# Performance work log

Hardware: AMD Instinct MI355X
Metric: run time of the kernel (lower is better)

The kernel has to match this reference:

```python
import jax, jax.numpy as jnp
import numpy as np

B, W, N, K = 8, 16, 40, 10
DN = DL = 128
DE = 128
H = 4
NEG_SLOPE = 0.2


def _build_graph():
    # per-graph ring adjacency: i -> (i+d) % N for d=1..K, in dense_to_sparse order (src-major, dst ascending)
    src0, dst0 = [], []
    for i in range(N):
        ds = sorted(((i + d) % N) for d in range(1, K + 1))
        src0 += [i] * K
        dst0 += ds
    src0 = np.asarray(src0)
    dst0 = np.asarray(dst0)
    G = B * W
    Epg = N * K
    offs = np.arange(G)[:, None] * N
    node_adj = np.stack([(src0[None] + offs).reshape(-1), (dst0[None] + offs).reshape(-1)])
    # line graph: for each node, pair every incoming edge with every outgoing edge (torch repeat/tile order)
    a0, a1, fe = [], [], []
    for num in range(N):
        inc = np.nonzero(dst0 == num)[0]
        out = np.nonzero(src0 == num)[0]
        a0.append(np.repeat(inc, out.size))
        a1.append(np.tile(out, inc.size))
        fe.append(np.full(inc.size * out.size, num))
    a0, a1, fe = np.concatenate(a0), np.concatenate(a1), np.concatenate(fe)
    keep = a0 != a1  # remove_self_loops (no-op here, kept for fidelity)
    a0, a1, fe = a0[keep], a1[keep], fe[keep]
    eoffs = np.arange(G)[:, None] * Epg
    edge_adj = np.stack([(a0[None] + eoffs).reshape(-1), (a1[None] + eoffs).reshape(-1)])
    edge_efea = (fe[None] + offs).reshape(-1)
    return node_adj, edge_adj, edge_efea


def setup_inputs() -> dict:
    key = jax.random.key(0)
    node_adj, edge_adj, edge_efea = _build_graph()
    Epg = N * K
    D1 = DN + DL
    ks = jax.random.split(key, 16)

    def lin(k, fi, fo):
        return jax.random.normal(k, (fi, fo), jnp.float32) / np.sqrt(fi).astype(np.float32)

    return dict(
        x_node=jax.random.normal(ks[0], (B, W, N, DN), jnp.float32),
        x_trace=jax.random.normal(ks[1], (B, W, Epg, DE), jnp.float32),
        x_log=jax.random.normal(ks[2], (B, W, N, DL), jnp.float32),
        node_adj=jnp.asarray(node_adj, jnp.int32),
        edge_adj=jnp.asarray(edge_adj, jnp.int32),
        edge_efea=jnp.asarray(edge_efea, jnp.int32),
        Wl1=lin(ks[3], D1, D1), bl1=jnp.zeros((D1,), jnp.float32),
        Wr1=lin(ks[4], D1, D1), br1=jnp.zeros((D1,), jnp.float32),
        We1=lin(ks[5], DE, D1), be1=jnp.zeros((D1,), jnp.float32),
        att1=jax.random.normal(ks[6], (H, D1 // H), jnp.float32) / np.sqrt(D1 // H).astype(np.float32),
        bias1=jnp.zeros((D1,), jnp.float32),
        Wl2=lin(ks[7], DE, DE), bl2=jnp.zeros((DE,), jnp.float32),
        Wr2=lin(ks[8], DE, DE), br2=jnp.zeros((DE,), jnp.float32),
        We2=lin(ks[9], D1, DE), be2=jnp.zeros((DE,), jnp.float32),
        att2=jax.random.normal(ks[10], (H, DE // H), jnp.float32) / np.sqrt(DE // H).astype(np.float32),
        bias2=jnp.zeros((DE,), jnp.float32),
    )


def _gatv2(x, edge_index, edge_attr, Wl, bl, Wr, br, We, be, att, bias, heads):
    """PyG GATv2Conv (eval mode, add_self_loops=False, concat heads)."""
    n = x.shape[0]
    HC = Wl.shape[1]
    C = HC // heads
    xl = (x @ Wl + bl).reshape(n, heads, C)  # source transform
    xr = (x @ Wr + br).reshape(n, heads, C)  # target transform
    src, dst = edge_index[0], edge_index[1]
    ea = (edge_attr @ We + be).reshape(-1, heads, C)
    m = jax.nn.leaky_relu(xl[src] + xr[dst] + ea, NEG_SLOPE)  # [E,H,C]
    logits = jnp.einsum('ehc,hc->eh', m, att)
    # segment softmax over incoming edges per target node
    mx = jax.ops.segment_max(logits, dst, num_segments=n)
    mx = jnp.where(jnp.isfinite(mx), mx, 0.0)
    ex = jnp.exp(logits - mx[dst])
    den = jax.ops.segment_sum(ex, dst, num_segments=n)
    alpha = ex / (den[dst] + 1e-16)
    out = jax.ops.segment_sum(alpha[:, :, None] * xl[src], dst, num_segments=n)  # [n,H,C]
    return out.reshape(n, HC) + bias


def reference(x_node, x_trace, x_log, node_adj, edge_adj, edge_efea,
              Wl1, bl1, Wr1, br1, We1, be1, att1, bias1,
              Wl2, bl2, Wr2, br2, We2, be2, att2, bias2):
    b, w, n, dn = x_node.shape
    dl = x_log.shape[-1]
    node = jnp.concatenate([x_node, x_log], axis=-1).reshape(-1, dn + dl)  # [G*N, Dn+Dl]
    trace = x_trace.reshape(-1, x_trace.shape[-1])                          # [G*Epg, De]
    node = _gatv2(node, node_adj, trace, Wl1, bl1, Wr1, br1, We1, be1, att1, bias1, H)
    trace = _gatv2(trace, edge_adj, node[edge_efea], Wl2, bl2, Wr2, br2, We2, be2, att2, bias2, H)
    x_node_o = node[:, :dn].reshape(b, w, n, dn)
    x_trace_o = trace.reshape(b, w, -1, trace.shape[-1])
    x_log_o = node[:, dn:].reshape(b, w, n, dl)
    return (x_node_o, x_trace_o, x_log_o)
```

## Files before the change

### kernel.cpp

```cpp
#include <hip/hip_runtime.h>
#include <hip/hip_bf16.h>

#define D1 256
#define DE 128
#define KDEG 10
#define NPG 40
#define EPG 400
#define LOG2E 1.44269504088896340736f

typedef __attribute__((ext_vector_type(8))) short short8;
typedef __attribute__((ext_vector_type(4))) float f32x4;

static inline int cdiv(size_t a, int b) { return (int)((a + b - 1) / b); }
static inline size_t al256(size_t x) { return (x + 255) & ~(size_t)255; }

__device__ __forceinline__ short f2b(float x) {
  __hip_bfloat16 h = __float2bfloat16(x);
  return *reinterpret_cast<short*>(&h);
}

__device__ __forceinline__ short8 cvt8(const float* __restrict__ src) {
  float4 v0 = *(const float4*)src;
  float4 v1 = *(const float4*)(src + 4);
  short8 t;
  t[0] = f2b(v0.x); t[1] = f2b(v0.y); t[2] = f2b(v0.z); t[3] = f2b(v0.w);
  t[4] = f2b(v1.x); t[5] = f2b(v1.y); t[6] = f2b(v1.z); t[7] = f2b(v1.w);
  return t;
}

__global__ __launch_bounds__(256) void k_setup(const float* __restrict__ xn,
                                               const float* __restrict__ xlg,
                                               const float* __restrict__ xtr,
                                               const float* __restrict__ Wl1,
                                               const float* __restrict__ Wr1,
                                               const float* __restrict__ We1,
                                               const float* __restrict__ Wl2,
                                               const float* __restrict__ Wr2,
                                               const float* __restrict__ We2,
                                               const float* __restrict__ bl1,
                                               const float* __restrict__ br1,
                                               const float* __restrict__ be1,
                                               const float* __restrict__ bl2,
                                               const float* __restrict__ br2,
                                               const int* __restrict__ adj,
                                               int* __restrict__ cnt,
                                               int* __restrict__ inc,
                                               short* __restrict__ Xb,
                                               short* __restrict__ xtr_b,
                                               short* __restrict__ WT12,
                                               short* __restrict__ WTall,
                                               short* __restrict__ We2T,
                                               float* __restrict__ blr1,
                                               float* __restrict__ bfull,
                                               int NN, int NE) {
  size_t idx = (size_t)blockIdx.x * 256 + threadIdx.x;
  size_t n;
  n = (size_t)NN * 32;
  if (idx < n) {
    int row = (int)(idx >> 5), q = (int)(idx & 31);
    const float* src = (q < 16) ? &xn[(size_t)row * 128 + q * 8]
                                : &xlg[(size_t)row * 128 + (q - 16) * 8];
    *(short8*)&Xb[(size_t)row * 256 + q * 8] = cvt8(src);
    return;
  }
  idx -= n;
  n = (size_t)NE * 16;
  if (idx < n) {
    *(short8*)&xtr_b[idx * 8] = cvt8(&xtr[idx * 8]);
    return;
  }
  idx -= n;
  n = 512 * 256;
  if (idx < n) {
    int nn = (int)(idx >> 8), k = (int)(idx & 255);
    float v = (nn < 256) ? Wl1[(size_t)k * 256 + nn] : Wr1[(size_t)k * 256 + (nn - 256)];
    WT12[idx] = f2b(v);
    return;
  }
  idx -= n;
  n = 512 * 128;
  if (idx < n) {
    int nn = (int)(idx >> 7), k = (int)(idx & 127);
    float v;
    if (nn < 256)      v = We1[(size_t)k * 256 + nn];
    else if (nn < 384) v = Wl2[(size_t)k * 128 + (nn - 256)];
    else               v = Wr2[(size_t)k * 128 + (nn - 384)];
    WTall[idx] = f2b(v);
    return;
  }
  idx -= n;
  n = 128 * 256;
  if (idx < n) {
    int nn = (int)(idx >> 8), k = (int)(idx & 255);
    We2T[idx] = f2b(We2[(size_t)k * 128 + nn]);
    return;
  }
  idx -= n;
  n = 512;
  if (idx < n) { blr1[idx] = (idx < 256) ? bl1[idx] : br1[idx - 256]; return; }
  idx -= n;
  n = 512;
  if (idx < n) {
    bfull[idx] = (idx < 256) ? be1[idx] : (idx < 384 ? bl2[idx - 256] : br2[idx - 384]);
    return;
  }
  idx -= n;
  n = (size_t)NE;
  if (idx < n) {
    int dst = adj[NE + idx];
    int slot = atomicAdd(&cnt[dst], 1);
    inc[dst * KDEG + slot] = (int)idx;
  }
}

__global__ __launch_bounds__(256) void k_gemm_dual(const short* __restrict__ Xb,
                                                   const short* __restrict__ WT12,
                                                   const float* __restrict__ blr1,
                                                   float* __restrict__ xlr1,
                                                   const short* __restrict__ xtr_b,
                                                   const short* __restrict__ WTl2,
                                                   const float* __restrict__ bia2,
                                                   float* __restrict__ pool2,
                                                   int NN, int NE) {
  __shared__ __align__(16) short As[64][40];
  __shared__ __align__(16) short Bs[64][40];
  const int tid = threadIdx.x;
  const int wave = tid >> 6, lane = tid & 63;
  const int quad = lane >> 4, l16 = lane & 15;
  const short *A, *WT;
  const float* bias;
  float* C;
  int K, N, m0, n0;
  {
    int bid = blockIdx.x;
    if (bid < 8 * (NN / 64)) {
      A = Xb; WT = WT12; bias = blr1; C = xlr1; K = 256; N = 512;
      n0 = (bid & 7) * 64; m0 = (bid >> 3) * 64;
    } else {
      bid -= 8 * (NN / 64);
      A = xtr_b; WT = WTl2; bias = bia2; C = pool2; K = 128; N = 256;
      n0 = (bid & 3) * 64; m0 = (bid >> 2) * 64;
    }
  }
  const int wm = (wave & 1) * 32, wn = (wave >> 1) * 32;
  const int r = tid >> 2, kc = (tid & 3) << 3;
  f32x4 acc[2][2] = {};
  short8 pa = *(const short8*)&A[(size_t)(m0 + r) * K + kc];
  short8 pb = *(const short8*)&WT[(size_t)(n0 + r) * K + kc];
  for (int k0 = 0; k0 < K; k0 += 32) {
    *(short8*)&As[r][kc] = pa;
    *(short8*)&Bs[r][kc] = pb;
    __syncthreads();
    if (k0 + 32 < K) {
      pa = *(const short8*)&A[(size_t)(m0 + r) * K + (k0 + 32 + kc)];
      pb = *(const short8*)&WT[(size_t)(n0 + r) * K + (k0 + 32 + kc)];
    }
    short8 af[2], bf[2];
    #pragma unroll
    for (int mt = 0; mt < 2; ++mt)
      af[mt] = *(const short8*)&As[wm + mt * 16 + l16][quad << 3];
    #pragma unroll
    for (int nt = 0; nt < 2; ++nt)
      bf[nt] = *(const short8*)&Bs[wn + nt * 16 + l16][quad << 3];
    #pragma unroll
    for (int mt = 0; mt < 2; ++mt)
      #pragma unroll
      for (int nt = 0; nt < 2; ++nt)
        acc[mt][nt] = __builtin_amdgcn_mfma_f32_16x16x32_bf16(
            af[mt], bf[nt], acc[mt][nt], 0, 0, 0);
    __syncthreads();
  }
  #pragma unroll
  for (int nt = 0; nt < 2; ++nt) {
    int col = n0 + wn + nt * 16 + l16;
    float bs = bias[col];
    #pragma unroll
    for (int mt = 0; mt < 2; ++mt) {
      int row = m0 + wm + mt * 16 + (quad << 2);
      #pragma unroll
      for (int rr = 0; rr < 2 * 2; ++rr)
        if (rr < 4) C[(size_t)(row + rr) * N + col] = acc[mt][nt][rr] + bs;
    }
  }
}

__global__ __launch_bounds__(256) void k_gemm_mfma64(const short* __restrict__ A,
                                                     const short* __restrict__ WT,
                                                     const float* __restrict__ bias,
                                                     float* __restrict__ C,
                                                     int M, int K, int N) {
  __shared__ __align__(16) short As[64][40];
  __shared__ __align__(16) short Bs[64][40];
  const int tid = threadIdx.x;
  const int wave = tid >> 6, lane = tid & 63;
  const int quad = lane >> 4, l16 = lane & 15;
  const int m0 = blockIdx.y * 64, n0 = blockIdx.x * 64;
  const int wm = (wave & 1) * 32, wn = (wave >> 1) * 32;
  const int r = tid >> 2, kc = (tid & 3) << 3;
  f32x4 acc[2][2] = {};
  short8 pa = *(const short8*)&A[(size_t)(m0 + r) * K + kc];
  short8 pb = *(const short8*)&WT[(size_t)(n0 + r) * K + kc];
  for (int k0 = 0; k0 < K; k0 += 32) {
    *(short8*)&As[r][kc] = pa;
    *(short8*)&Bs[r][kc] = pb;
    __syncthreads();
    if (k0 + 32 < K) {
      pa = *(const short8*)&A[(size_t)(m0 + r) * K + (k0 + 32 + kc)];
      pb = *(const short8*)&WT[(size_t)(n0 + r) * K + (k0 + 32 + kc)];
    }
    short8 af[2], bf[2];
    #pragma unroll
    for (int mt = 0; mt < 2; ++mt)
      af[mt] = *(const short8*)&As[wm + mt * 16 + l16][quad << 3];
    #pragma unroll
    for (int nt = 0; nt < 2; ++nt)
      bf[nt] = *(const short8*)&Bs[wn + nt * 16 + l16][quad << 3];
    #pragma unroll
    for (int mt = 0; mt < 2; ++mt)
      #pragma unroll
      for (int nt = 0; nt < 2; ++nt)
        acc[mt][nt] = __builtin_amdgcn_mfma_f32_16x16x32_bf16(
            af[mt], bf[nt], acc[mt][nt], 0, 0, 0);
    __syncthreads();
  }
  #pragma unroll
  for (int nt = 0; nt < 2; ++nt) {
    int col = n0 + wn + nt * 16 + l16;
    float bs = bias[col];
    #pragma unroll
    for (int mt = 0; mt < 2; ++mt) {
      int row = m0 + wm + mt * 16 + (quad << 2);
      #pragma unroll
      for (int rr = 0; rr < 4; ++rr)
        C[(size_t)(row + rr) * N + col] = acc[mt][nt][rr] + bs;
    }
  }
}

__global__ __launch_bounds__(256) void k_logit(const short* __restrict__ A,
                                               const short* __restrict__ WT,
                                               const float* __restrict__ bfull,
                                               const float* __restrict__ att1,
                                               const int* __restrict__ adj,
                                               const float* __restrict__ xlr1,
                                               float* __restrict__ logit1,
                                               int NE) {
  const int K = 128;
  struct SmemGemm { short As[128][40]; short Bs[64][40]; };
  struct SmemEpi  { int sdst[128]; float sxl[14][68]; float sxr[NPG][68]; };
  __shared__ __align__(16) union { SmemGemm g; SmemEpi e; } sm;
  const int tid = threadIdx.x;
  const int wave = tid >> 6, lane = tid & 63;
  const int quad = lane >> 4, l16 = lane & 15;
  int bid = blockIdx.x;
  int l = (bid & 7) * ((int)gridDim.x >> 3) + (bid >> 3);
  const int n0 = (l & 3) << 6;
  const int m0 = (l >> 2) << 7;
  const int wm = wave * 32;
  const int ra0 = tid >> 2, ra1 = ra0 + 64;
  const int kc = (tid & 3) << 3;
  f32x4 acc[2][4] = {};
  short8 pa0 = *(const short8*)&A[(size_t)(m0 + ra0) * K + kc];
  short8 pa1 = *(const short8*)&A[(size_t)(m0 + ra1) * K + kc];
  short8 pb  = *(const short8*)&WT[(size_t)(n0 + ra0) * K + kc];
  for (int k0 = 0; k0 < K; k0 += 32) {
    *(short8*)&sm.g.As[ra0][kc] = pa0;
    *(short8*)&sm.g.As[ra1][kc] = pa1;
    *(short8*)&sm.g.Bs[ra0][kc] = pb;
    __syncthreads();
    if (k0 + 32 < K) {
      pa0 = *(const short8*)&A[(size_t)(m0 + ra0) * K + (k0 + 32 + kc)];
      pa1 = *(const short8*)&A[(size_t)(m0 + ra1) * K + (k0 + 32 + kc)];
      pb  = *(const short8*)&WT[(size_t)(n0 + ra0) * K + (k0 + 32 + kc)];
    }
    short8 af[2], bf[4];
    #pragma unroll
    for (int mt = 0; mt < 2; ++mt)
      af[mt] = *(const short8*)&sm.g.As[wm + mt * 16 + l16][quad << 3];
    #pragma unroll
    for (int nt = 0; nt < 4; ++nt)
      bf[nt] = *(const short8*)&sm.g.Bs[nt * 16 + l16][quad << 3];
    #pragma unroll
    for (int mt = 0; mt < 2; ++mt)
      #pragma unroll
      for (int nt = 0; nt < 4; ++nt)
        acc[mt][nt] = __builtin_amdgcn_mfma_f32_16x16x32_bf16(
            af[mt], bf[nt], acc[mt][nt], 0, 0, 0);
    __syncthreads();
  }
  const int gl = m0 / EPG;
  const int gh = (m0 + 127) / EPG;
  const int slo = m0 / KDEG;
  const int nrl = (m0 + 127) / KDEG - slo + 1;
  if (tid < 128) sm.e.sdst[tid] = adj[NE + m0 + tid];
  for (int s = tid; s < nrl * 64; s += 256) {
    int row = s >> 6, c = s & 63;
    sm.e.sxl[row][c] = xlr1[(size_t)(slo + row) * 512 + n0 + c];
  }
  const int h = n0 >> 6;
  float attv[4], bev[4];
  int ccl[4];
  #pragma unroll
  for (int nt = 0; nt < 4; ++nt) {
    int col = n0 + nt * 16 + l16;
    ccl[nt] = col - n0;
    attv[nt] = att1[col] * LOG2E;
    bev[nt] = bfull[col];
  }
  for (int g = gl; g <= gh; ++g) {
    __syncthreads();
    for (int s = tid; s < NPG * 64; s += 256) {
      int row = s >> 6, c = s & 63;
      sm.e.sxr[row][c] = xlr1[(size_t)(g * NPG + row) * 512 + 256 + n0 + c];
    }
    __syncthreads();
    const int elo = g * EPG, ehi = elo + EPG;
    #pragma unroll
    for (int mt = 0; mt < 2; ++mt) {
      #pragma unroll
      for (int r = 0; r < 4; ++r) {
        int le = wm + mt * 16 + (quad << 2) + r;
        int e = m0 + le;
        if (e < elo || e >= ehi) continue;
        int srow = e / KDEG - slo;
        int d = sm.e.sdst[le];
        int drow = d - g * NPG;
        float p = 0.f;
        #pragma unroll
        for (int nt = 0; nt < 4; ++nt) {
          float v = acc[mt][nt][r] + bev[nt] + sm.e.sxl[srow][ccl[nt]]
                  + sm.e.sxr[drow][ccl[nt]];
          v = (v > 0.f) ? v : 0.2f * v;
          p += v * attv[nt];
        }
        p += __shfl_xor(p, 1, 64);
        p += __shfl_xor(p, 2, 64);
        p += __shfl_xor(p, 4, 64);
        p += __shfl_xor(p, 8, 64);
        if (l16 == 0) {
          logit1[(size_t)e * 4 + h] = exp2f(p);
        }
      }
    }
  }
}

__global__ __launch_bounds__(256) void k_agg1(const int* __restrict__ adj,
                                              const int* __restrict__ inc,
                                              const float* __restrict__ xlr1,
                                              const float* __restrict__ logit1,
                                              const float* __restrict__ bias1,
                                              short* __restrict__ nodeoutb,
                                              float* __restrict__ out_node,
                                              float* __restrict__ out_log) {
  int u = blockIdx.x, c = threadIdx.x;
  __shared__ int se[KDEG], ssrc[KDEG];
  __shared__ float slg[KDEG * 4];
  if (c < KDEG) se[c] = inc[u * KDEG + c];
  __syncthreads();
  if (c < KDEG) ssrc[c] = adj[se[c]];
  else if (c >= 64 && c < 64 + KDEG * 4) {
    int t = c - 64;
    slg[t] = logit1[(size_t)se[t >> 2] * 4 + (t & 3)];
  }
  __syncthreads();
  int h = c >> 6;
  float den = 0.f;
  #pragma unroll
  for (int j = 0; j < KDEG; ++j) den += slg[j * 4 + h];
  float rden = 1.f / (den + 1e-16f);
  float acc = 0.f;
  #pragma unroll
  for (int j = 0; j < KDEG; ++j)
    acc += slg[j * 4 + h] * xlr1[(size_t)ssrc[j] * 512 + c];
  float val = acc * rden + bias1[c];
  nodeoutb[(size_t)u * D1 + c] = f2b(val);
  if (c < 128) out_node[(size_t)u * 128 + c] = val;
  else         out_log[(size_t)u * 128 + (c - 128)] = val;
}

__global__ __launch_bounds__(256) void k_gat2_v4(const int* __restrict__ eadj,
                                                 const int* __restrict__ efea,
                                                 const float* __restrict__ pool2,
                                                 const float* __restrict__ nproj,
                                                 const float* __restrict__ att2,
                                                 const float* __restrict__ bias2,
                                                 float* __restrict__ out_trace,
                                                 int NL) {
  int gi = blockIdx.x;
  size_t le0 = (size_t)gi * 100;
  int t = threadIdx.x;
  const int wave = t >> 6, lane = t & 63;
  __shared__ int ein[KDEG], eout[KDEG], nvs;
  __shared__ float xs[KDEG][132];
  __shared__ float rs[KDEG][132];
  __shared__ float as_[DE];
  __shared__ float exs[400];
  __shared__ float rdn[40];
  if (t < KDEG)          ein[t] = eadj[le0 + (size_t)t * KDEG];
  else if (t < 2 * KDEG) eout[t - KDEG] = eadj[(size_t)NL + le0 + (t - KDEG)];
  else if (t == 255)     nvs = efea[le0];
  __syncthreads();
  int nv = nvs;
  for (int s = t; s < 320; s += 256) {
    int j = s >> 5, q = (s & 31) << 2;
    *(float4*)&xs[j][q] = *(const float4*)&pool2[(size_t)ein[j] * 256 + q];
    float4 tr4 = *(const float4*)&pool2[(size_t)eout[j] * 256 + 128 + q];
    float4 ea4 = *(const float4*)&nproj[(size_t)nv * DE + q];
    float4 r;
    r.x = tr4.x + ea4.x; r.y = tr4.y + ea4.y;
    r.z = tr4.z + ea4.z; r.w = tr4.w + ea4.w;
    *(float4*)&rs[j][q] = r;
  }
  if (t < 32) {
    float4 a4 = *(const float4*)&att2[t << 2];
    float4 o;
    o.x = a4.x * LOG2E; o.y = a4.y * LOG2E;
    o.z = a4.z * LOG2E; o.w = a4.w * LOG2E;
    *(float4*)&as_[t << 2] = o;
  }
  __syncthreads();
  {
    int h = wave;
    const float* aa = &as_[h << 5];
    for (int idx = lane; idx < 100; idx += 64) {
      int j = idx / 10;
      int o = idx - j * 10;
      const float* xa = &xs[j][h << 5];
      const float* ra = &rs[o][h << 5];
      float p = 0.f;
      #pragma unroll
      for (int i = 0; i < 32; i += 4) {
        float4 xv = *(const float4*)&xa[i];
        float4 rv = *(const float4*)&ra[i];
        float4 av = *(const float4*)&aa[i];
        float v;
        v = xv.x + rv.x; v = (v > 0.f) ? v : 0.2f * v; p += v * av.x;
        v = xv.y + rv.y; v = (v > 0.f) ? v : 0.2f * v; p += v * av.y;
        v = xv.z + rv.z; v = (v > 0.f) ? v : 0.2f * v; p += v * av.z;
        v = xv.w + rv.w; v = (v > 0.f) ? v : 0.2f * v; p += v * av.w;
      }
      exs[(j * 10 + o) * 4 + h] = exp2f(p);
    }
  }
  __syncthreads();
  if (t < 40) {
    float d = 0.f;
    #pragma unroll
    for (int j = 0; j < KDEG; ++j) d += exs[(j * 10 + (t >> 2)) * 4 + (t & 3)];
    rdn[t] = 1.f / d;
  }
  __syncthreads();
  {
    int c = t & 127, h = c >> 5, oh = (t >> 7) * 5;
    float bsv = bias2[c];
    #pragma unroll
    for (int oo = 0; oo < 5; ++oo) {
      int o = oh + oo;
      float acc = 0.f;
      #pragma unroll
      for (int j = 0; j < KDEG; ++j)
        acc += exs[(j * 10 + o) * 4 + h] * xs[j][c];
      out_trace[(size_t)eout[o] * DE + c] = acc * rdn[o * 4 + h] + bsv;
    }
  }
}

extern "C" void kernel_launch(void* const* d_in, const int* in_sizes, int n_in,
                              void* d_out, int out_size, void* d_ws, size_t ws_size,
                              hipStream_t stream) {
  const float* x_node   = (const float*)d_in[0];
  const float* x_trace  = (const float*)d_in[1];
  const float* x_log    = (const float*)d_in[2];
  const int*   node_adj = (const int*)d_in[3];
  const int*   edge_adj = (const int*)d_in[4];
  const int*   edge_efea= (const int*)d_in[5];
  const float* Wl1 = (const float*)d_in[6];
  const float* bl1 = (const float*)d_in[7];
  const float* Wr1 = (const float*)d_in[8];
  const float* br1 = (const float*)d_in[9];
  const float* We1 = (const float*)d_in[10];
  const float* be1 = (const float*)d_in[11];
  const float* att1 = (const float*)d_in[12];
  const float* bias1 = (const float*)d_in[13];
  const float* Wl2 = (const float*)d_in[14];
  const float* bl2 = (const float*)d_in[15];
  const float* Wr2 = (const float*)d_in[16];
  const float* br2 = (const float*)d_in[17];
  const float* We2 = (const float*)d_in[18];
  const float* be2 = (const float*)d_in[19];
  const float* att2 = (const float*)d_in[20];
  const float* bias2 = (const float*)d_in[21];

  const int NN = in_sizes[0] / 128;
  const int NE = in_sizes[1] / 128;
  const int NL = in_sizes[5];

  char* p = (char*)d_ws;
  float* pool2   = (float*)p; p += al256((size_t)NE * 256 * 4);
  float* xlr1    = (float*)p; p += al256((size_t)NN * 512 * 4);
  short* Xb      = (short*)p; p += al256((size_t)NN * D1 * 2);
  short* xtr_b   = (short*)p; p += al256((size_t)NE * DE * 2);
  short* nodeoutb= (short*)p; p += al256((size_t)NN * D1 * 2);
  float* nproj   = (float*)p; p += al256((size_t)NN * DE * 4);
  float* logit1  = (float*)p; p += al256((size_t)NE * 4 * 4);
  int*   inc     = (int*)p;   p += al256((size_t)NN * KDEG * 4);
  int*   cnt     = (int*)p;   p += al256((size_t)NN * 4);
  short* WT12    = (short*)p; p += al256((size_t)512 * 256 * 2);
  short* WTall   = (short*)p; p += al256((size_t)512 * 128 * 2);
  short* We2T    = (short*)p; p += al256((size_t)128 * 256 * 2);
  float* blr1    = (float*)p; p += al256(512 * 4);
  float* bfull   = (float*)p; p += al256(512 * 4);
  (void)ws_size;

  float* out_node  = (float*)d_out;
  float* out_trace = out_node + (size_t)NN * 128;
  float* out_log   = out_trace + (size_t)NE * 128;

  hipMemsetAsync(cnt, 0, (size_t)NN * 4, stream);
  {
    size_t total = (size_t)NN * 32 + (size_t)NE * 16 +
                   512 * 256 + 512 * 128 + 128 * 256 + 512 + 512 + (size_t)NE;
    k_setup<<<cdiv(total, 256), 256, 0, stream>>>(x_node, x_log, x_trace,
                                                  Wl1, Wr1, We1, Wl2, Wr2, We2,
                                                  bl1, br1, be1, bl2, br2,
                                                  node_adj, cnt, inc,
                                                  Xb, xtr_b,
                                                  WT12, WTall, We2T, blr1, bfull,
                                                  NN, NE);
  }

  k_gemm_dual<<<8 * (NN / 64) + 4 * (NE / 64), 256, 0, stream>>>(
      Xb, WT12, blr1, xlr1,
      xtr_b, WTall + (size_t)256 * 128, bfull + 256, pool2, NN, NE);

  k_logit<<<4 * (NE / 128), 256, 0, stream>>>(xtr_b, WTall, bfull, att1,
                                              node_adj, xlr1, logit1, NE);

  k_agg1<<<NN, 256, 0, stream>>>(node_adj, inc, xlr1, logit1, bias1,
                                 nodeoutb, out_node, out_log);

  k_gemm_mfma64<<<dim3(DE / 64, NN / 64), 256, 0, stream>>>(nodeoutb, We2T, be2,
                                                            nproj, NN, D1, DE);

  k_gat2_v4<<<NN, 256, 0, stream>>>(edge_adj, edge_efea, pool2, nproj,
                                    att2, bias2, out_trace, NL);
}
```

Measured before the change: 219.7 us.

## Deepen 64x64 GEMM K-tile to 64 and remap agg1 blocks across XCDs

The 64x64 MFMA GEMM now stages a K-slice of 64 per iteration, with two 16-byte loads per thread and two MFMA sub-steps, which halves the number of barrier-separated loop iterations and doubles the loads in flight. The LDS padding grows to match. Separately, k_agg1 permutes blockIdx so that consecutive nodes are spread across the eight XCDs, and a redundant bounds check in the other GEMM epilogue is removed. The cost is more LDS and registers per block, and the remap assumes the grid size is divisible by 8 and K is a multiple of 64.

Result: no change. 217.0 us (-1.3%).

```diff
diff --git a/kernel.cpp b/kernel.cpp
--- a/kernel.cpp
+++ b/kernel.cpp
@@ -178,8 +178,8 @@
     for (int mt = 0; mt < 2; ++mt) {
       int row = m0 + wm + mt * 16 + (quad << 2);
       #pragma unroll
-      for (int rr = 0; rr < 2 * 2; ++rr)
-        if (rr < 4) C[(size_t)(row + rr) * N + col] = acc[mt][nt][rr] + bs;
+      for (int rr = 0; rr < 4; ++rr)
+        C[(size_t)(row + rr) * N + col] = acc[mt][nt][rr] + bs;
     }
   }
 }
@@ -189,38 +189,47 @@
                                                      const float* __restrict__ bias,
                                                      float* __restrict__ C,
                                                      int M, int K, int N) {
-  __shared__ __align__(16) short As[64][40];
-  __shared__ __align__(16) short Bs[64][40];
+  __shared__ __align__(16) short As[64][72];
+  __shared__ __align__(16) short Bs[64][72];
   const int tid = threadIdx.x;
   const int wave = tid >> 6, lane = tid & 63;
   const int quad = lane >> 4, l16 = lane & 15;
   const int m0 = blockIdx.y * 64, n0 = blockIdx.x * 64;
   const int wm = (wave & 1) * 32, wn = (wave >> 1) * 32;
-  const int r = tid >> 2, kc = (tid & 3) << 3;
+  const int r = tid >> 2, kc = (tid & 3) << 4;
   f32x4 acc[2][2] = {};
-  short8 pa = *(const short8*)&A[(size_t)(m0 + r) * K + kc];
-  short8 pb = *(const short8*)&WT[(size_t)(n0 + r) * K + kc];
-  for (int k0 = 0; k0 < K; k0 += 32) {
-    *(short8*)&As[r][kc] = pa;
-    *(short8*)&Bs[r][kc] = pb;
-    __syncthreads();
-    if (k0 + 32 < K) {
-      pa = *(const short8*)&A[(size_t)(m0 + r) * K + (k0 + 32 + kc)];
-      pb = *(const short8*)&WT[(size_t)(n0 + r) * K + (k0 + 32 + kc)];
-    }
-    short8 af[2], bf[2];
-    #pragma unroll
-    for (int mt = 0; mt < 2; ++mt)
-      af[mt] = *(const short8*)&As[wm + mt * 16 + l16][quad << 3];
-    #pragma unroll
-    for (int nt = 0; nt < 2; ++nt)
-      bf[nt] = *(const short8*)&Bs[wn + nt * 16 + l16][quad << 3];
-    #pragma unroll
-    for (int mt = 0; mt < 2; ++mt)
+  short8 pa0 = *(const short8*)&A[(size_t)(m0 + r) * K + kc];
+  short8 pa1 = *(const short8*)&A[(size_t)(m0 + r) * K + kc + 8];
+  short8 pb0 = *(const short8*)&WT[(size_t)(n0 + r) * K + kc];
+  short8 pb1 = *(const short8*)&WT[(size_t)(n0 + r) * K + kc + 8];
+  for (int k0 = 0; k0 < K; k0 += 64) {
+    *(short8*)&As[r][kc] = pa0;
+    *(short8*)&As[r][kc + 8] = pa1;
+    *(short8*)&Bs[r][kc] = pb0;
+    *(short8*)&Bs[r][kc + 8] = pb1;
+    __syncthreads();
+    if (k0 + 64 < K) {
+      pa0 = *(const short8*)&A[(size_t)(m0 + r) * K + (k0 + 64 + kc)];
+      pa1 = *(const short8*)&A[(size_t)(m0 + r) * K + (k0 + 64 + kc + 8)];
+      pb0 = *(const short8*)&WT[(size_t)(n0 + r) * K + (k0 + 64 + kc)];
+      pb1 = *(const short8*)&WT[(size_t)(n0 + r) * K + (k0 + 64 + kc + 8)];
+    }
+    #pragma unroll
+    for (int kk = 0; kk < 2; ++kk) {
+      short8 af[2], bf[2];
+      #pragma unroll
+      for (int mt = 0; mt < 2; ++mt)
+        af[mt] = *(const short8*)&As[wm + mt * 16 + l16][kk * 32 + (quad << 3)];
       #pragma unroll
       for (int nt = 0; nt < 2; ++nt)
-        acc[mt][nt] = __builtin_amdgcn_mfma_f32_16x16x32_bf16(
-            af[mt], bf[nt], acc[mt][nt], 0, 0, 0);
+        bf[nt] = *(const short8*)&Bs[wn + nt * 16 + l16][kk * 32 + (quad << 3)];
+      #pragma unroll
+      for (int mt = 0; mt < 2; ++mt)
+        #pragma unroll
+        for (int nt = 0; nt < 2; ++nt)
+          acc[mt][nt] = __builtin_amdgcn_mfma_f32_16x16x32_bf16(
+              af[mt], bf[nt], acc[mt][nt], 0, 0, 0);
+    }
     __syncthreads();
   }
   #pragma unroll
@@ -353,7 +362,8 @@
                                               short* __restrict__ nodeoutb,
                                               float* __restrict__ out_node,
                                               float* __restrict__ out_log) {
-  int u = blockIdx.x, c = threadIdx.x;
+  int u = (blockIdx.x & 7) * ((int)gridDim.x >> 3) + (blockIdx.x >> 3);
+  int c = threadIdx.x;
   __shared__ int se[KDEG], ssrc[KDEG];
   __shared__ float slg[KDEG * 4];
   if (c < KDEG) se[c] = inc[u * KDEG + c];
```
